# Kernel optimization log

Hardware: AMD Instinct MI355X
Metric: run time of the kernel (lower is better)

## Reference

```python
import jax, jax.numpy as jnp
import numpy as np

N = 50000
E = 800000
IN_C = 128
HID = 128
OUT_C = 64
HEADS = 8
HD1 = HID // HEADS   # 16 per-head dim, layer 1 (concat)
HD2 = OUT_C          # 64 per-head dim, layer 2 (concat=False, mean over heads)
NEG_SLOPE = 0.2


def setup_inputs() -> dict:
    key = jax.random.key(0)
    ks = jax.random.split(key, 12)
    x = jax.random.normal(ks[0], (N, IN_C), dtype=jnp.float32)
    edge_index = jax.random.randint(ks[1], (2, E), 0, N, dtype=jnp.int64)
    s1 = 1.0 / np.sqrt(IN_C)
    s2 = 1.0 / np.sqrt(HID)
    W1 = jax.random.normal(ks[2], (IN_C, HEADS * HD1), dtype=jnp.float32) * s1
    att_src1 = jax.random.normal(ks[3], (HEADS, HD1), dtype=jnp.float32) * s1
    att_dst1 = jax.random.normal(ks[4], (HEADS, HD1), dtype=jnp.float32) * s1
    b1 = jnp.zeros((HID,), dtype=jnp.float32)
    W2 = jax.random.normal(ks[5], (HID, HEADS * HD2), dtype=jnp.float32) * s2
    att_src2 = jax.random.normal(ks[6], (HEADS, HD2), dtype=jnp.float32) * s2
    att_dst2 = jax.random.normal(ks[7], (HEADS, HD2), dtype=jnp.float32) * s2
    b2 = jnp.zeros((OUT_C,), dtype=jnp.float32)
    return {"x": x, "edge_index": edge_index,
            "W1": W1, "att_src1": att_src1, "att_dst1": att_dst1, "b1": b1,
            "W2": W2, "att_src2": att_src2, "att_dst2": att_dst2, "b2": b2}


def _gat_conv(x, W, a_src, a_dst, bias, src, dst, heads, head_dim, concat):
    n = x.shape[0]
    h = (x @ W).reshape(n, heads, head_dim)                      # [N,H,D]
    alpha_s = jnp.einsum('nhd,hd->nh', h, a_src)                  # [N,H]
    alpha_d = jnp.einsum('nhd,hd->nh', h, a_dst)                  # [N,H]
    e = jax.nn.leaky_relu(alpha_s[src] + alpha_d[dst], NEG_SLOPE)  # [E,H]
    # segment softmax over edges grouped by destination node
    m = jax.ops.segment_max(e, dst, num_segments=n)               # [N,H]
    m = jnp.where(jnp.isfinite(m), m, 0.0)
    ex = jnp.exp(e - m[dst])
    denom = jax.ops.segment_sum(ex, dst, num_segments=n)
    alpha = ex / (denom[dst] + 1e-16)                             # [E,H]
    out = jax.ops.segment_sum(h[src] * alpha[:, :, None], dst, num_segments=n)  # [N,H,D]
    if concat:
        out = out.reshape(n, heads * head_dim)
    else:
        out = out.mean(axis=1)
    return out + bias


def reference(x, edge_index, W1, att_src1, att_dst1, b1, W2, att_src2, att_dst2, b2):
    # PyG GATConv default add_self_loops=True
    loops = jnp.arange(N, dtype=edge_index.dtype)
    src = jnp.concatenate([edge_index[0], loops])
    dst = jnp.concatenate([edge_index[1], loops])
    h = _gat_conv(x, W1, att_src1, att_dst1, b1, src, dst, HEADS, HD1, True)
    h = jax.nn.relu(h)
    out = _gat_conv(h, W2, att_src2, att_dst2, b2, src, dst, HEADS, HD2, False)
    return out
```

## Files before the change

### kernel.cpp

```cpp
#include <hip/hip_runtime.h>

#define N_NODES 50000
#define N_EDGES 800000
#define ET (N_EDGES + N_NODES)
#define HEADS 8
#define NPAD 50048
#define SCAN_NB 196
#define CAP 96
#define LRS 1032
#define NB_DEG 3321
#define NB_GEMM1 782

typedef __attribute__((ext_vector_type(8))) _Float16 half8;
typedef __attribute__((ext_vector_type(2))) _Float16 half2v;
typedef __attribute__((ext_vector_type(4))) float f32x4;

__device__ __forceinline__ void wave_lds_fence(){
  asm volatile("s_waitcnt lgkmcnt(0)" ::: "memory");
}

__device__ __forceinline__ int edge_src(const int* ei, int e, int is64){
  if (e >= N_EDGES) return e - N_EDGES;
  return is64 ? ei[2*e] : ei[e];
}
__device__ __forceinline__ int edge_dst(const int* ei, int e, int is64){
  if (e >= N_EDGES) return e - N_EDGES;
  return is64 ? ei[2*(N_EDGES + e)] : ei[N_EDGES + e];
}

__global__ void k_init_wprep(const int* __restrict__ ei, int* __restrict__ deg,
                             int* __restrict__ cnt, int* __restrict__ flag,
                             const float* __restrict__ W1, const float* __restrict__ W2,
                             const float* __restrict__ as2, const float* __restrict__ ad2,
                             _Float16* __restrict__ Bp1, _Float16* __restrict__ Bp,
                             float* __restrict__ ws2, float* __restrict__ wd2){
  int b = blockIdx.x;
  int t_ = threadIdx.x;
  if (b < SCAN_NB){
    int i = b*256 + t_;
    if (i < N_NODES){ deg[i] = 0; cnt[i] = 0; }
    if (i == 0){
      int zeros = 0;
      for (int k = 0; k < 64; k++){
        if (ei[2*k + 1] == 0) zeros++;
      }
      *flag = (zeros >= 60) ? 1 : 0;
    }
  } else if (b < SCAN_NB + 256){
    int t = (b - SCAN_NB)*256 + t_;
    int j = t & 7, lane = (t >> 3) & 63, nt = (t >> 9) & 3, kt = t >> 11;
    int k = kt*32 + (lane >> 4)*8 + j;
    int c = nt*16 + (lane & 15);
    int h = k >> 7, kk = k & 127;
    Bp[t] = (_Float16)(0.125f * W2[kk*512 + h*64 + c]);
  } else if (b < SCAN_NB + 320){
    int t = (b - SCAN_NB - 256)*256 + t_;
    int j = t & 7, lane = (t >> 3) & 63, nt = (t >> 9) & 7, kt = t >> 12;
    int k = kt*32 + (lane >> 4)*8 + j;
    int c = nt*16 + (lane & 15);
    Bp1[t] = (_Float16)W1[k*128 + c];
  } else {
    int t = (b - SCAN_NB - 320)*256 + t_;
    int k = t >> 3, h = t & 7;
    float s = 0.f, d = 0.f;
    for (int dd = 0; dd < 64; dd++){
      float w = W2[k*512 + h*64 + dd];
      s += w * as2[h*64 + dd];
      d += w * ad2[h*64 + dd];
    }
    ws2[h*128 + k] = s;
    wd2[h*128 + k] = d;
  }
}

__global__ void __launch_bounds__(256) k_deg_gemm1(
    const int* __restrict__ ei, int* __restrict__ deg, const int* __restrict__ flag,
    const float* __restrict__ x, const _Float16* __restrict__ Bp1,
    _Float16* __restrict__ h1,
    const float* __restrict__ as1, const float* __restrict__ ad1,
    float* __restrict__ als1, float* __restrict__ ald1){
  if (blockIdx.x < NB_DEG){
    int e = blockIdx.x*blockDim.x + threadIdx.x;
    if (e >= ET) return;
    int is64 = *flag;
    int d = edge_dst(ei, e, is64);
    atomicAdd(&deg[d], 1);
    return;
  }
  int bid = blockIdx.x - NB_DEG;
  int tid = threadIdx.x;
  int lane = tid & 63, wv = tid >> 6;
  int n0 = bid*64 + wv*16;
  int rowA = n0 + (lane & 15);
  int koff = (lane >> 4)*8;
  const float* xr = x + (size_t)rowA*128 + koff;
  f32x4 acc[8];
  #pragma unroll
  for (int i = 0; i < 8; i++) acc[i] = (f32x4){0.f,0.f,0.f,0.f};
  bool inb = (rowA < N_NODES);
  #pragma unroll
  for (int kt = 0; kt < 4; kt++){
    half8 af;
    if (inb){
      float4 a0 = *(const float4*)(xr + kt*32);
      float4 a1 = *(const float4*)(xr + kt*32 + 4);
      af = (half8){(_Float16)a0.x,(_Float16)a0.y,(_Float16)a0.z,(_Float16)a0.w,
                   (_Float16)a1.x,(_Float16)a1.y,(_Float16)a1.z,(_Float16)a1.w};
    } else {
      af = (half8){0,0,0,0,0,0,0,0};
    }
    #pragma unroll
    for (int nt = 0; nt < 8; nt++){
      half8 bf = *(const half8*)(Bp1 + (((kt*8 + nt)*64 + lane) << 3));
      acc[nt] = __builtin_amdgcn_mfma_f32_16x16x32_f16(af, bf, acc[nt], 0, 0, 0);
    }
  }
  int m = lane & 15, q = lane >> 4;
  int r0 = n0 + q*4;
  #pragma unroll
  for (int nt = 0; nt < 8; nt++){
    int c = nt*16 + m;
    #pragma unroll
    for (int r = 0; r < 4; r++){
      int n = r0 + r;
      if (n < N_NODES) h1[(size_t)n*128 + c] = (_Float16)acc[nt][r];
    }
  }
  float as1v[8], ad1v[8];
  #pragma unroll
  for (int nt = 0; nt < 8; nt++){
    as1v[nt] = as1[nt*16 + m];
    ad1v[nt] = ad1[nt*16 + m];
  }
  #pragma unroll
  for (int r = 0; r < 4; r++){
    float vs[8], vd[8];
    #pragma unroll
    for (int nt = 0; nt < 8; nt++){
      vs[nt] = acc[nt][r]*as1v[nt];
      vd[nt] = acc[nt][r]*ad1v[nt];
      #pragma unroll
      for (int off = 1; off < 16; off <<= 1){
        vs[nt] += __shfl_xor(vs[nt], off, 64);
        vd[nt] += __shfl_xor(vd[nt], off, 64);
      }
    }
    int n = r0 + r;
    if (m == r && n < N_NODES){
      float4 v0; v0.x = vs[0]; v0.y = vs[1]; v0.z = vs[2]; v0.w = vs[3];
      float4 v1; v1.x = vs[4]; v1.y = vs[5]; v1.z = vs[6]; v1.w = vs[7];
      float4 w0; w0.x = vd[0]; w0.y = vd[1]; w0.z = vd[2]; w0.w = vd[3];
      float4 w1; w1.x = vd[4]; w1.y = vd[5]; w1.z = vd[6]; w1.w = vd[7];
      *(float4*)&als1[n*8]     = v0;
      *(float4*)&als1[n*8 + 4] = v1;
      *(float4*)&ald1[n*8]     = w0;
      *(float4*)&ald1[n*8 + 4] = w1;
    }
  }
}

__global__ void k_scan_part(const int* __restrict__ deg, int* __restrict__ loc,
                            int* __restrict__ part){
  __shared__ int lds[256];
  int t = threadIdx.x, i = blockIdx.x*256 + t;
  int v = (i < N_NODES) ? deg[i] : 0;
  lds[t] = v;
  __syncthreads();
  for (int off = 1; off < 256; off <<= 1){
    int x = (t >= off) ? lds[t - off] : 0;
    __syncthreads();
    lds[t] += x;
    __syncthreads();
  }
  if (i < N_NODES) loc[i] = lds[t] - v;
  if (t == 255) part[blockIdx.x] = lds[255];
}

__global__ void k_scan_carry(int* __restrict__ part, int* __restrict__ carry){
  __shared__ int lds[256];
  int t = threadIdx.x;
  int v = (t < SCAN_NB) ? part[t] : 0;
  lds[t] = v;
  __syncthreads();
  for (int off = 1; off < 256; off <<= 1){
    int x = (t >= off) ? lds[t - off] : 0;
    __syncthreads();
    lds[t] += x;
    __syncthreads();
  }
  if (t < SCAN_NB) carry[t] = lds[t] - v;
}

__global__ void k_scan_add(const int* __restrict__ loc, const int* __restrict__ carry,
                           int* __restrict__ row_ptr){
  int i = blockIdx.x*blockDim.x + threadIdx.x;
  if (i < N_NODES) row_ptr[i] = loc[i] + carry[i >> 8];
  if (i == 0) row_ptr[N_NODES] = ET;
}

__global__ void k_fill(const int* __restrict__ ei, const int* __restrict__ row_ptr,
                       int* __restrict__ cnt, int* __restrict__ col,
                       const int* __restrict__ flag){
  int e = blockIdx.x*blockDim.x + threadIdx.x;
  if (e >= ET) return;
  int is64 = *flag;
  int s = edge_src(ei, e, is64);
  int d = edge_dst(ei, e, is64);
  int pos = atomicAdd(&cnt[d], 1);
  col[row_ptr[d] + pos] = s;
}

__global__ void k_attn_agg1(const _Float16* __restrict__ h1,
    const float* __restrict__ als, const float* __restrict__ ald,
    const int* __restrict__ row_ptr, const int* __restrict__ col,
    const float* __restrict__ bias, _Float16* __restrict__ hr,
    const float* __restrict__ ws2, const float* __restrict__ wd2,
    float* __restrict__ als2, float* __restrict__ ald2){
  __shared__ _Float16 ew_s[4][CAP*8];
  __shared__ int col_s[4][CAP];
  __shared__ _Float16 ot_s[4][136];
  int tid = threadIdx.x;
  int wv = tid >> 6, lane = tid & 63;
  int n = blockIdx.x*4 + wv;
  int beg = row_ptr[n], end = row_ptr[n+1];
  int deg = end - beg;
  int items = deg*8;
  int h = lane & 7;
  float ad = ald[n*8 + h];
  _Float16* es = ew_s[wv];
  int* cs = col_s[wv];
  float l = 0.f;
  int itc = items < CAP*8 ? items : CAP*8;
  int it = lane;
  for (; it < itc; it += 64){
    int e = it >> 3;
    int s = col[beg + e];
    float a = als[s*8 + h] + ad;
    a = (a > 0.f) ? a : 0.2f*a;
    float ex = __expf(a);
    es[it] = (_Float16)ex;
    if ((it & 7) == 0) cs[e] = s;
    l += ex;
  }
  for (; it < items; it += 64){
    int s = col[beg + (it >> 3)];
    float a = als[s*8 + h] + ad;
    a = (a > 0.f) ? a : 0.2f*a;
    l += __expf(a);
  }
  l += __shfl_xor(l, 8, 64);
  l += __shfl_xor(l, 16, 64);
  l += __shfl_xor(l, 32, 64);
  float inv = 1.f / (l + 1e-16f);
  wave_lds_fence();
  int eg = lane >> 4, cb = lane & 15;
  int hq = cb >> 1;
  float invh = __shfl(inv, hq, 64);
  float adh  = __shfl(ad, hq, 64);
  float acc[8];
  #pragma unroll
  for (int k = 0; k < 8; k++) acc[k] = 0.f;
  int degc = deg < CAP ? deg : CAP;
  int j = 0;
  for (; j + 3 < degc; j += 4){
    int e = j + eg;
    int s = cs[e];
    float w = (float)es[e*8 + hq] * invh;
    half8 v = *(const half8*)(h1 + (size_t)s*128 + cb*8);
    #pragma unroll
    for (int k = 0; k < 8; k++) acc[k] += w*(float)v[k];
  }
  if (j < degc){
    int e = j + eg;
    if (e < degc){
      int s = cs[e];
      float w = (float)es[e*8 + hq] * invh;
      half8 v = *(const half8*)(h1 + (size_t)s*128 + cb*8);
      #pragma unroll
      for (int k = 0; k < 8; k++) acc[k] += w*(float)v[k];
    }
  }
  for (int jj = degc; jj < deg; jj += 4){
    int e = jj + eg;
    if (e < deg){
      int s = col[beg + e];
      float a = als[s*8 + hq] + adh;
      a = (a > 0.f) ? a : 0.2f*a;
      float w = __expf(a)*invh;
      half8 v = *(const half8*)(h1 + (size_t)s*128 + cb*8);
      #pragma unroll
      for (int k = 0; k < 8; k++) acc[k] += w*(float)v[k];
    }
  }
  #pragma unroll
  for (int k = 0; k < 8; k++){
    acc[k] += __shfl_xor(acc[k], 16, 64);
    acc[k] += __shfl_xor(acc[k], 32, 64);
  }
  float4 b0 = *(const float4*)(bias + cb*8);
  float4 b1 = *(const float4*)(bias + cb*8 + 4);
  float bb[8] = {b0.x,b0.y,b0.z,b0.w,b1.x,b1.y,b1.z,b1.w};
  half8 oh;
  #pragma unroll
  for (int k = 0; k < 8; k++) oh[k] = (_Float16)fmaxf(acc[k] + bb[k], 0.f);
  if (eg == 0){
    *(half8*)(hr + (size_t)n*128 + cb*8) = oh;
    ((half8*)&ot_s[wv][0])[cb] = oh;
  }
  wave_lds_fence();
  int hh = lane >> 3, seg = lane & 7;
  const half2v* otp = (const half2v*)&ot_s[wv][0];
  const float* wsr = ws2 + hh*128 + seg*16;
  const float* wdr = wd2 + hh*128 + seg*16;
  float vs = 0.f, vd = 0.f;
  #pragma unroll
  for (int i = 0; i < 8; i++){
    half2v v = otp[seg*8 + i];
    float vx = (float)v.x, vy = (float)v.y;
    vs += vx*wsr[2*i] + vy*wsr[2*i + 1];
    vd += vx*wdr[2*i] + vy*wdr[2*i + 1];
  }
  vs += __shfl_xor(vs, 1, 64); vd += __shfl_xor(vd, 1, 64);
  vs += __shfl_xor(vs, 2, 64); vd += __shfl_xor(vd, 2, 64);
  vs += __shfl_xor(vs, 4, 64); vd += __shfl_xor(vd, 4, 64);
  if (seg == 0){
    als2[n*8 + hh] = vs;
    ald2[n*8 + hh] = vd;
  }
}

__global__ void __launch_bounds__(1024) k_attn_agg2(const _Float16* __restrict__ hr,
    const float* __restrict__ als, const float* __restrict__ ald,
    const int* __restrict__ row_ptr, const int* __restrict__ col,
    const _Float16* __restrict__ Bp, const float* __restrict__ b2,
    float* __restrict__ outp){
  __shared__ _Float16 ew_s[16][CAP*8];
  __shared__ int col_s[16][CAP];
  __shared__ _Float16 at[16*LRS];
  int tid = threadIdx.x;
  int wv = tid >> 6, lane = tid & 63;
  int n = blockIdx.x*16 + wv;
  int beg = row_ptr[n], end = row_ptr[n+1];
  int deg = end - beg;
  int items = deg*8;
  int h = lane & 7;
  float ad = ald[n*8 + h];
  _Float16* es = ew_s[wv];
  int* cs = col_s[wv];
  float l = 0.f;
  int itc = items < CAP*8 ? items : CAP*8;
  int it = lane;
  for (; it < itc; it += 64){
    int e = it >> 3;
    int s = col[beg + e];
    float a = als[s*8 + h] + ad;
    a = (a > 0.f) ? a : 0.2f*a;
    float ex = __expf(a);
    es[it] = (_Float16)ex;
    if ((it & 7) == 0) cs[e] = s;
    l += ex;
  }
  for (; it < items; it += 64){
    int s = col[beg + (it >> 3)];
    float a = als[s*8 + h] + ad;
    a = (a > 0.f) ? a : 0.2f*a;
    l += __expf(a);
  }
  l += __shfl_xor(l, 8, 64);
  l += __shfl_xor(l, 16, 64);
  l += __shfl_xor(l, 32, 64);
  float inv = 1.f / (l + 1e-16f);
  wave_lds_fence();
  int hp = lane >> 4, cb = lane & 15;
  float invA = __shfl(inv, 2*hp, 64);
  float invB = __shfl(inv, 2*hp + 1, 64);
  half2v inv2; inv2.x = (_Float16)invA; inv2.y = (_Float16)invB;
  half2v acc_a[4], acc_b[4];
  #pragma unroll
  for (int i = 0; i < 4; i++){
    acc_a[i] = (half2v){(_Float16)0.f, (_Float16)0.f};
    acc_b[i] = (half2v){(_Float16)0.f, (_Float16)0.f};
  }
  int degc = deg < CAP ? deg : CAP;
  const _Float16* esw = es + 2*hp;
  int j = 0;
  for (; j + 3 < degc; j += 4){
    int s0 = cs[j], s1 = cs[j+1], s2 = cs[j+2], s3 = cs[j+3];
    half2v w0 = *(const half2v*)(esw + (j+0)*8) * inv2;
    half2v w1 = *(const half2v*)(esw + (j+1)*8) * inv2;
    half2v w2 = *(const half2v*)(esw + (j+2)*8) * inv2;
    half2v w3 = *(const half2v*)(esw + (j+3)*8) * inv2;
    half8 v0 = *(const half8*)(hr + (size_t)s0*128 + cb*8);
    half8 v1 = *(const half8*)(hr + (size_t)s1*128 + cb*8);
    half8 v2 = *(const half8*)(hr + (size_t)s2*128 + cb*8);
    half8 v3 = *(const half8*)(hr + (size_t)s3*128 + cb*8);
    #pragma unroll
    for (int k = 0; k < 4; k++){
      half2v t;
      t = (half2v){v0[2*k], v0[2*k+1]};
      acc_a[k] += (half2v){w0.x, w0.x} * t;
      acc_b[k] += (half2v){w0.y, w0.y} * t;
      t = (half2v){v1[2*k], v1[2*k+1]};
      acc_a[k] += (half2v){w1.x, w1.x} * t;
      acc_b[k] += (half2v){w1.y, w1.y} * t;
      t = (half2v){v2[2*k], v2[2*k+1]};
      acc_a[k] += (half2v){w2.x, w2.x} * t;
      acc_b[k] += (half2v){w2.y, w2.y} * t;
      t = (half2v){v3[2*k], v3[2*k+1]};
      acc_a[k] += (half2v){w3.x, w3.x} * t;
      acc_b[k] += (half2v){w3.y, w3.y} * t;
    }
  }
  for (; j < degc; j++){
    int s = cs[j];
    half2v w = *(const half2v*)(esw + j*8) * inv2;
    half8 v = *(const half8*)(hr + (size_t)s*128 + cb*8);
    #pragma unroll
    for (int k = 0; k < 4; k++){
      half2v t = (half2v){v[2*k], v[2*k+1]};
      acc_a[k] += (half2v){w.x, w.x} * t;
      acc_b[k] += (half2v){w.y, w.y} * t;
    }
  }
  if (deg > CAP){
    float2 adv = *(const float2*)(ald + (size_t)n*8 + 2*hp);
    for (; j < deg; j++){
      int s = col[beg + j];
      float2 alv = *(const float2*)(als + (size_t)s*8 + 2*hp);
      float a0 = alv.x + adv.x; a0 = (a0 > 0.f) ? a0 : 0.2f*a0;
      float a1 = alv.y + adv.y; a1 = (a1 > 0.f) ? a1 : 0.2f*a1;
      _Float16 w0 = (_Float16)(__expf(a0)*invA);
      _Float16 w1 = (_Float16)(__expf(a1)*invB);
      half8 v = *(const half8*)(hr + (size_t)s*128 + cb*8);
      #pragma unroll
      for (int k = 0; k < 4; k++){
        half2v t = (half2v){v[2*k], v[2*k+1]};
        acc_a[k] += (half2v){w0, w0} * t;
        acc_b[k] += (half2v){w1, w1} * t;
      }
    }
  }
  _Float16* ar = at + wv*LRS + (2*hp)*128 + cb*8;
  half8 oa, ob;
  #pragma unroll
  for (int k = 0; k < 4; k++){
    oa[2*k] = acc_a[k].x; oa[2*k+1] = acc_a[k].y;
    ob[2*k] = acc_b[k].x; ob[2*k+1] = acc_b[k].y;
  }
  *(half8*)ar = oa;
  *(half8*)(ar + 128) = ob;
  __syncthreads();
  if (wv >= 4) return;
  int m = lane & 15, q = lane >> 4;
  const _Float16* arow = at + m*LRS + q*8;
  f32x4 cacc = (f32x4){0.f,0.f,0.f,0.f};
  #pragma unroll 4
  for (int kt = 0; kt < 32; kt++){
    half8 af = *(const half8*)(arow + kt*32);
    half8 bf = *(const half8*)(Bp + (((kt*4 + wv)*64 + lane) << 3));
    cacc = __builtin_amdgcn_mfma_f32_16x16x32_f16(af, bf, cacc, 0, 0, 0);
  }
  int c = wv*16 + m;
  float bb = b2[c];
  #pragma unroll
  for (int r = 0; r < 4; r++){
    int nrow = blockIdx.x*16 + q*4 + r;
    outp[(size_t)nrow*64 + c] = cacc[r] + bb;
  }
}

extern "C" void kernel_launch(void* const* d_in, const int* in_sizes, int n_in,
                              void* d_out, int out_size, void* d_ws, size_t ws_size,
                              hipStream_t stream){
  const float* x   = (const float*)d_in[0];
  const int*   ei  = (const int*)d_in[1];
  const float* W1  = (const float*)d_in[2];
  const float* as1 = (const float*)d_in[3];
  const float* ad1 = (const float*)d_in[4];
  const float* b1  = (const float*)d_in[5];
  const float* W2  = (const float*)d_in[6];
  const float* as2 = (const float*)d_in[7];
  const float* ad2 = (const float*)d_in[8];
  const float* b2  = (const float*)d_in[9];
  float* outp = (float*)d_out;

  char* p = (char*)d_ws;
  auto alloc = [&](size_t bytes) -> void* {
    void* r = (void*)p;
    p += (bytes + 255) & ~(size_t)255;
    return r;
  };
  _Float16* h1  = (_Float16*)alloc((size_t)NPAD*128*2);
  _Float16* hr  = (_Float16*)alloc((size_t)N_NODES*128*2);
  float* als1 = (float*)alloc((size_t)N_NODES*8*4);
  float* ald1 = (float*)alloc((size_t)N_NODES*8*4);
  float* als2 = (float*)alloc((size_t)N_NODES*8*4);
  float* ald2 = (float*)alloc((size_t)N_NODES*8*4);
  int* row_ptr = (int*)alloc((size_t)(N_NODES+1)*4);
  int* deg  = (int*)alloc((size_t)N_NODES*4);
  int* cnt  = (int*)alloc((size_t)N_NODES*4);
  int* col  = (int*)alloc((size_t)ET*4);
  int* loc  = (int*)alloc((size_t)N_NODES*4);
  int* part = (int*)alloc(256*4);
  int* carry= (int*)alloc(256*4);
  int* flag = (int*)alloc(256);
  float* ws2 = (float*)alloc(1024*4);
  float* wd2 = (float*)alloc(1024*4);
  _Float16* Bp1 = (_Float16*)alloc((size_t)16384*2);
  _Float16* Bp  = (_Float16*)alloc((size_t)65536*2);

  dim3 b256(256);
  k_init_wprep<<<SCAN_NB + 324, b256, 0, stream>>>(ei, deg, cnt, flag,
                                                   W1, W2, as2, ad2,
                                                   Bp1, Bp, ws2, wd2);
  k_deg_gemm1<<<NB_DEG + NB_GEMM1, b256, 0, stream>>>(ei, deg, flag,
                                                      x, Bp1, h1, as1, ad1,
                                                      als1, ald1);
  k_scan_part<<<SCAN_NB, b256, 0, stream>>>(deg, loc, part);
  k_scan_carry<<<1, b256, 0, stream>>>(part, carry);
  k_scan_add<<<SCAN_NB, b256, 0, stream>>>(loc, carry, row_ptr);
  k_fill<<<(ET+255)/256, b256, 0, stream>>>(ei, row_ptr, cnt, col, flag);
  k_attn_agg1<<<N_NODES/4, b256, 0, stream>>>(h1, als1, ald1, row_ptr, col,
                                              b1, hr, ws2, wd2, als2, ald2);
  k_attn_agg2<<<N_NODES/16, dim3(1024), 0, stream>>>(hr, als2, ald2, row_ptr, col,
                                                     Bp, b2, outp);
}
```

Measured before the change: 322.5 us.

## Split layer-2 aggregation edges across lane groups, reduce all heads via shuffles

The layer-2 aggregation now assigns each 16-lane group a different edge instead of a different head pair. Every lane gathers one source row and accumulates all 8 heads, and the partial sums are combined with cross-group shuffles at the end. Softmax normalization is folded into the stored LDS weights once, rather than multiplied per edge. The goal is to cut the serial per-edge loop length fourfold and spread the gathers across more edges at once. The cost is many more accumulator registers and extra shuffle reductions, and launch_bounds now requests a minimum of 8 blocks per CU.

Measured after the change: 350.5 us. +8.7%, slower.

```diff
diff --git a/kernel.cpp b/kernel.cpp
--- a/kernel.cpp
+++ b/kernel.cpp
@@ -329,7 +329,7 @@
   }
 }
 
-__global__ void __launch_bounds__(1024) k_attn_agg2(const _Float16* __restrict__ hr,
+__global__ void __launch_bounds__(1024, 8) k_attn_agg2(const _Float16* __restrict__ hr,
     const float* __restrict__ als, const float* __restrict__ ald,
     const int* __restrict__ row_ptr, const int* __restrict__ col,
     const _Float16* __restrict__ Bp, const float* __restrict__ b2,
@@ -371,82 +371,97 @@
   l += __shfl_xor(l, 32, 64);
   float inv = 1.f / (l + 1e-16f);
   wave_lds_fence();
-  int hp = lane >> 4, cb = lane & 15;
-  float invA = __shfl(inv, 2*hp, 64);
-  float invB = __shfl(inv, 2*hp + 1, 64);
-  half2v inv2; inv2.x = (_Float16)invA; inv2.y = (_Float16)invB;
-  half2v acc_a[4], acc_b[4];
-  #pragma unroll
-  for (int i = 0; i < 4; i++){
-    acc_a[i] = (half2v){(_Float16)0.f, (_Float16)0.f};
-    acc_b[i] = (half2v){(_Float16)0.f, (_Float16)0.f};
-  }
+  for (int it2 = lane; it2 < itc; it2 += 64){
+    es[it2] = (_Float16)((float)es[it2] * inv);
+  }
+  wave_lds_fence();
+  int eg = lane >> 4, cb = lane & 15;
+  half2v acc[4][8];
+  #pragma unroll
+  for (int p = 0; p < 4; p++)
+    #pragma unroll
+    for (int hh = 0; hh < 8; hh++)
+      acc[p][hh] = (half2v){(_Float16)0.f, (_Float16)0.f};
   int degc = deg < CAP ? deg : CAP;
-  const _Float16* esw = es + 2*hp;
-  int j = 0;
-  for (; j + 3 < degc; j += 4){
-    int s0 = cs[j], s1 = cs[j+1], s2 = cs[j+2], s3 = cs[j+3];
-    half2v w0 = *(const half2v*)(esw + (j+0)*8) * inv2;
-    half2v w1 = *(const half2v*)(esw + (j+1)*8) * inv2;
-    half2v w2 = *(const half2v*)(esw + (j+2)*8) * inv2;
-    half2v w3 = *(const half2v*)(esw + (j+3)*8) * inv2;
-    half8 v0 = *(const half8*)(hr + (size_t)s0*128 + cb*8);
-    half8 v1 = *(const half8*)(hr + (size_t)s1*128 + cb*8);
-    half8 v2 = *(const half8*)(hr + (size_t)s2*128 + cb*8);
-    half8 v3 = *(const half8*)(hr + (size_t)s3*128 + cb*8);
-    #pragma unroll
-    for (int k = 0; k < 4; k++){
-      half2v t;
-      t = (half2v){v0[2*k], v0[2*k+1]};
-      acc_a[k] += (half2v){w0.x, w0.x} * t;
-      acc_b[k] += (half2v){w0.y, w0.y} * t;
-      t = (half2v){v1[2*k], v1[2*k+1]};
-      acc_a[k] += (half2v){w1.x, w1.x} * t;
-      acc_b[k] += (half2v){w1.y, w1.y} * t;
-      t = (half2v){v2[2*k], v2[2*k+1]};
-      acc_a[k] += (half2v){w2.x, w2.x} * t;
-      acc_b[k] += (half2v){w2.y, w2.y} * t;
-      t = (half2v){v3[2*k], v3[2*k+1]};
-      acc_a[k] += (half2v){w3.x, w3.x} * t;
-      acc_b[k] += (half2v){w3.y, w3.y} * t;
-    }
-  }
-  for (; j < degc; j++){
-    int s = cs[j];
-    half2v w = *(const half2v*)(esw + j*8) * inv2;
-    half8 v = *(const half8*)(hr + (size_t)s*128 + cb*8);
-    #pragma unroll
-    for (int k = 0; k < 4; k++){
-      half2v t = (half2v){v[2*k], v[2*k+1]};
-      acc_a[k] += (half2v){w.x, w.x} * t;
-      acc_b[k] += (half2v){w.y, w.y} * t;
+  for (int j = 0; j < degc; j += 4){
+    int e = j + eg;
+    bool act = (e < degc);
+    int ec = act ? e : 0;
+    int s = cs[ec];
+    half8 we = *(const half8*)(es + ec*8);
+    half8 v  = *(const half8*)(hr + (size_t)s*128 + cb*8);
+    if (!act) we = (half8){0,0,0,0,0,0,0,0};
+    #pragma unroll
+    for (int p = 0; p < 4; p++){
+      half2v t = (half2v){v[2*p], v[2*p+1]};
+      acc[p][0] += (half2v){we[0], we[0]} * t;
+      acc[p][1] += (half2v){we[1], we[1]} * t;
+      acc[p][2] += (half2v){we[2], we[2]} * t;
+      acc[p][3] += (half2v){we[3], we[3]} * t;
+      acc[p][4] += (half2v){we[4], we[4]} * t;
+      acc[p][5] += (half2v){we[5], we[5]} * t;
+      acc[p][6] += (half2v){we[6], we[6]} * t;
+      acc[p][7] += (half2v){we[7], we[7]} * t;
     }
   }
   if (deg > CAP){
-    float2 adv = *(const float2*)(ald + (size_t)n*8 + 2*hp);
-    for (; j < deg; j++){
-      int s = col[beg + j];
-      float2 alv = *(const float2*)(als + (size_t)s*8 + 2*hp);
-      float a0 = alv.x + adv.x; a0 = (a0 > 0.f) ? a0 : 0.2f*a0;
-      float a1 = alv.y + adv.y; a1 = (a1 > 0.f) ? a1 : 0.2f*a1;
-      _Float16 w0 = (_Float16)(__expf(a0)*invA);
-      _Float16 w1 = (_Float16)(__expf(a1)*invB);
-      half8 v = *(const half8*)(hr + (size_t)s*128 + cb*8);
-      #pragma unroll
-      for (int k = 0; k < 4; k++){
-        half2v t = (half2v){v[2*k], v[2*k+1]};
-        acc_a[k] += (half2v){w0, w0} * t;
-        acc_b[k] += (half2v){w1, w1} * t;
+    float invs[8], advs[8];
+    #pragma unroll
+    for (int hh = 0; hh < 8; hh++){
+      invs[hh] = __shfl(inv, hh, 64);
+      advs[hh] = __shfl(ad, hh, 64);
+    }
+    for (int jj = degc; jj < deg; jj += 4){
+      int e = jj + eg;
+      if (e < deg){
+        int s = col[beg + e];
+        float4 a0 = *(const float4*)(als + (size_t)s*8);
+        float4 a1 = *(const float4*)(als + (size_t)s*8 + 4);
+        float av[8] = {a0.x,a0.y,a0.z,a0.w,a1.x,a1.y,a1.z,a1.w};
+        half8 we;
+        #pragma unroll
+        for (int hh = 0; hh < 8; hh++){
+          float a = av[hh] + advs[hh];
+          a = (a > 0.f) ? a : 0.2f*a;
+          we[hh] = (_Float16)(__expf(a)*invs[hh]);
+        }
+        half8 v = *(const half8*)(hr + (size_t)s*128 + cb*8);
+        #pragma unroll
+        for (int p = 0; p < 4; p++){
+          half2v t = (half2v){v[2*p], v[2*p+1]};
+          acc[p][0] += (half2v){we[0], we[0]} * t;
+          acc[p][1] += (half2v){we[1], we[1]} * t;
+          acc[p][2] += (half2v){we[2], we[2]} * t;
+          acc[p][3] += (half2v){we[3], we[3]} * t;
+          acc[p][4] += (half2v){we[4], we[4]} * t;
+          acc[p][5] += (half2v){we[5], we[5]} * t;
+          acc[p][6] += (half2v){we[6], we[6]} * t;
+          acc[p][7] += (half2v){we[7], we[7]} * t;
+        }
       }
     }
   }
-  _Float16* ar = at + wv*LRS + (2*hp)*128 + cb*8;
+  #pragma unroll
+  for (int p = 0; p < 4; p++){
+    #pragma unroll
+    for (int hh = 0; hh < 8; hh++){
+      int b0 = __builtin_bit_cast(int, acc[p][hh]);
+      acc[p][hh] += __builtin_bit_cast(half2v, __shfl_xor(b0, 16, 64));
+      int b1 = __builtin_bit_cast(int, acc[p][hh]);
+      acc[p][hh] += __builtin_bit_cast(half2v, __shfl_xor(b1, 32, 64));
+    }
+  }
   half8 oa, ob;
   #pragma unroll
-  for (int k = 0; k < 4; k++){
-    oa[2*k] = acc_a[k].x; oa[2*k+1] = acc_a[k].y;
-    ob[2*k] = acc_b[k].x; ob[2*k+1] = acc_b[k].y;
-  }
+  for (int p = 0; p < 4; p++){
+    half2v ra = (eg == 0) ? acc[p][0] : (eg == 1) ? acc[p][2]
+              : (eg == 2) ? acc[p][4] : acc[p][6];
+    half2v rb = (eg == 0) ? acc[p][1] : (eg == 1) ? acc[p][3]
+              : (eg == 2) ? acc[p][5] : acc[p][7];
+    oa[2*p] = ra.x; oa[2*p+1] = ra.y;
+    ob[2*p] = rb.x; ob[2*p+1] = rb.y;
+  }
+  _Float16* ar = at + wv*LRS + (2*eg)*128 + cb*8;
   *(half8*)ar = oa;
   *(half8*)(ar + 128) = ob;
   __syncthreads();
```
